# Performance work log

Measured on AMD Instinct MI355X. Metric: run time of the kernel, lower is better.

Reference implementation:

```python
import jax, jax.numpy as jnp
import numpy as np

B, S, H, NH = 32, 512, 768, 12
EC, EU = 4, 4
CAP = 1.0
DH = H // NH
CAPACITY = int(CAP * B / EC)  # Switch-style capacity per common expert


def setup_inputs() -> dict:
    key = jax.random.key(0)
    ks = jax.random.split(key, 10)
    s = 0.02
    E = EC + EU  # experts stacked: [0:EC]=common, [EC:]=unique
    return {
        "hidden_states": jax.random.normal(ks[0], (B, S, H), jnp.float32),
        "attention_mask": jnp.zeros((B, S), jnp.float32),  # additive mask
        "Wq": jax.random.normal(ks[1], (E, H, H), jnp.float32) * s,
        "bq": jnp.zeros((E, H), jnp.float32),
        "Wk": jax.random.normal(ks[2], (E, H, H), jnp.float32) * s,
        "bk": jnp.zeros((E, H), jnp.float32),
        "Wv": jax.random.normal(ks[3], (E, H, H), jnp.float32) * s,
        "bv": jnp.zeros((E, H), jnp.float32),
        "Wo": jax.random.normal(ks[4], (E, H, H), jnp.float32) * s,
        "bo": jnp.zeros((E, H), jnp.float32),
        "Wsc": jax.random.normal(ks[5], (H, EC), jnp.float32) * s,
        "bsc": jnp.zeros((EC,), jnp.float32),
        "Wsu": jax.random.normal(ks[6], (H, EU), jnp.float32) * s,
        "bsu": jnp.zeros((EU,), jnp.float32),
    }


def reference(hidden_states, attention_mask, Wq, bq, Wk, bk, Wv, bv, Wo, bo,
              Wsc, bsc, Wsu, bsu):
    # ---- common routing (per-sequence top-1 over mean-pooled tokens) ----
    h_mean = hidden_states.mean(axis=1)                       # [B,H]
    pc = jax.nn.softmax(h_mean @ Wsc + bsc, axis=-1)          # [B,EC]
    rc = jnp.argmax(pc, axis=-1)                              # [B]
    pc_max = jnp.max(pc, axis=-1)                             # [B]
    # capacity drop: within each expert keep the CAPACITY highest-prob seqs
    order = jnp.argsort(-pc_max)                              # global desc sort
    oh = jax.nn.one_hot(rc[order], EC, dtype=jnp.int32)       # [B,EC]
    rank = jnp.take_along_axis(jnp.cumsum(oh, axis=0), rc[order][:, None], 1)[:, 0]
    kept = jnp.zeros((B,), bool).at[order].set(rank <= CAPACITY)

    # ---- unique routing for dropped sequences (mean is per-sequence, so
    #      computing on the full batch and masking matches torch) ----
    pu = jax.nn.softmax(h_mean @ Wsu + bsu, axis=-1)          # [B,EU]
    ru = jnp.argmax(pu, axis=-1)
    pu_max = jnp.max(pu, axis=-1)

    # per-sequence expert index into stacked [EC+EU] expert params
    eidx = jnp.where(kept, rc, EC + ru)                       # [B]
    # scaling factor p/stop_grad(p): ==1 in fwd, routes grads to the gate
    scale = jnp.where(kept,
                      pc_max / jax.lax.stop_gradient(pc_max),
                      pu_max / jax.lax.stop_gradient(pu_max))

    # ---- gather-dispatch: per-sequence expert weights ----
    Wq_b, Wk_b, Wv_b, Wo_b = Wq[eidx], Wk[eidx], Wv[eidx], Wo[eidx]  # [B,H,H]
    bq_b, bk_b, bv_b, bo_b = bq[eidx], bk[eidx], bv[eidx], bo[eidx]  # [B,H]

    def heads(t):  # [B,S,H] -> [B,NH,S,DH]
        return t.reshape(B, S, NH, DH).transpose(0, 2, 1, 3)

    q = heads(jnp.einsum('bsh,bhd->bsd', hidden_states, Wq_b) + bq_b[:, None, :])
    k = heads(jnp.einsum('bsh,bhd->bsd', hidden_states, Wk_b) + bk_b[:, None, :])
    v = heads(jnp.einsum('bsh,bhd->bsd', hidden_states, Wv_b) + bv_b[:, None, :])

    scores = jnp.einsum('bhsd,bhtd->bhst', q, k) / np.float32(np.sqrt(DH))
    scores = scores + attention_mask[:, None, None, :]        # additive mask
    attn = jax.nn.softmax(scores, axis=-1)
    ctx = jnp.einsum('bhst,bhtd->bhsd', attn, v)
    ctx = ctx.transpose(0, 2, 1, 3).reshape(B, S, H)

    out = jnp.einsum('bsh,bhd->bsd', ctx, Wo_b) + bo_b[:, None, :]
    return out * scale[:, None, None]
```

## Files before the change

kernel.cpp:

```cpp
#include <hip/hip_runtime.h>
#include <hip/hip_bf16.h>

#define B_ 32
#define S_ 512
#define H_ 768
#define NH_ 12
#define DH_ 64
#define EC_ 4
#define CAPN_ 8

using short8  = __attribute__((ext_vector_type(8))) short;
using floatx4 = __attribute__((ext_vector_type(4))) float;
using uint2v  = __attribute__((ext_vector_type(2))) unsigned;
using bf16 = __hip_bfloat16;

#define VMCNT(n) asm volatile("s_waitcnt vmcnt(" #n ")" ::: "memory")

__device__ __forceinline__ void gl_lds16(const void* g, void* l) {
  __builtin_amdgcn_global_load_lds(
      (const __attribute__((address_space(1))) unsigned int*)g,
      (__attribute__((address_space(3))) unsigned int*)l, 16, 0, 0);
}

__device__ __forceinline__ unsigned pk2(float lo, float hi) {
  __hip_bfloat162 h = __float22bfloat162_rn(make_float2(lo, hi));
  unsigned r;
  __builtin_memcpy(&r, &h, 4);
  return r;
}

__global__ void k_prep(const float* __restrict__ X, bf16* __restrict__ Xh,
                       float* __restrict__ partial,
                       const float* __restrict__ Wq, const float* __restrict__ Wk,
                       const float* __restrict__ Wv, const float* __restrict__ Wo,
                       bf16* __restrict__ Wt) {
  __shared__ float tile[32][33];
  int f = blockIdx.x;
  if (f < 768) {
    int bx = f % 96, by = f / 96;
    int idx = bx * 256 + threadIdx.x;
    int b = idx / H_, h = idx - b * H_;
    int s0 = by * 64;
    size_t base = ((size_t)b * S_ + s0) * H_ + h;
    float sum = 0.f;
#pragma unroll 8
    for (int s = 0; s < 64; ++s) {
      float v = X[base + (size_t)s * H_];
      Xh[base + (size_t)s * H_] = __float2bfloat16(v);
      sum += v;
    }
    partial[(size_t)by * (B_ * H_) + idx] = sum;
  } else {
    int wid = f - 768;
    int z = wid / 576;
    int rem = wid - z * 576;
    int xx = rem / 24, yy = rem - xx * 24;
    const float* Wbase = (z < 8 ? Wq : z < 16 ? Wk : z < 24 ? Wv : Wo) + (size_t)(z & 7) * H_ * H_;
    int k0 = xx * 32, n0 = yy * 32;
    int tj = threadIdx.x & 31, ti = threadIdx.x >> 5;
#pragma unroll
    for (int r = 0; r < 4; ++r)
      tile[ti + r * 8][tj] = Wbase[(size_t)(k0 + ti + r * 8) * H_ + n0 + tj];
    __syncthreads();
    bf16* out = Wt + (size_t)z * H_ * H_;
#pragma unroll
    for (int r = 0; r < 4; ++r)
      out[(size_t)(n0 + ti + r * 8) * H_ + k0 + tj] = __float2bfloat16(tile[tj][ti + r * 8]);
  }
}

__global__ void k_mean_reduce(const float* __restrict__ partial, float* __restrict__ hmean) {
  int idx = blockIdx.x * 256 + threadIdx.x;
  float s = 0.f;
#pragma unroll
  for (int c = 0; c < 8; ++c) s += partial[(size_t)c * (B_ * H_) + idx];
  hmean[idx] = s * (1.f / 512.f);
}

__global__ void k_gate(const float* __restrict__ hmean,
                       const float* __restrict__ Wsc, const float* __restrict__ bsc,
                       const float* __restrict__ Wsu, const float* __restrict__ bsu,
                       float* __restrict__ logits) {
  int b = blockIdx.x;
  int t = threadIdx.x;
  int g = t >> 3, p = t & 7;
  const float* hm = hmean + (size_t)b * H_;
  const float* w;
  float bias;
  if (g < 4) { w = Wsc + g; bias = bsc[g]; }
  else       { w = Wsu + (g - 4); bias = bsu[g - 4]; }
  float acc = 0.f;
  for (int j = p; j < H_; j += 8) acc += hm[j] * w[j * 4];
  acc += __shfl_xor(acc, 1);
  acc += __shfl_xor(acc, 2);
  acc += __shfl_xor(acc, 4);
  if (p == 0) logits[b * 8 + g] = acc + bias;
}

__global__ void k_route2(const float* __restrict__ logits, int* __restrict__ eidx) {
  __shared__ float pcmax[B_];
  __shared__ int rc_s[B_], ru_s[B_];
  int t = threadIdx.x;
  if (t < B_) {
    float lg[8];
#pragma unroll
    for (int e = 0; e < 8; ++e) lg[e] = logits[t * 8 + e];
    float m = lg[0]; int a = 0;
    for (int e = 1; e < 4; ++e) if (lg[e] > m) { m = lg[e]; a = e; }
    float s = 0.f;
    for (int e = 0; e < 4; ++e) s += expf(lg[e] - m);
    pcmax[t] = 1.f / s;
    rc_s[t] = a;
    float mu = lg[4]; int au = 0;
    for (int e = 1; e < 4; ++e) if (lg[4 + e] > mu) { mu = lg[4 + e]; au = e; }
    ru_s[t] = au;
  }
  __syncthreads();
  if (t == 0) {
    bool used[B_], kept[B_];
    int cnt[EC_] = {0, 0, 0, 0};
    for (int i = 0; i < B_; ++i) used[i] = false;
    for (int i = 0; i < B_; ++i) {
      int best = 0; float bv = -1e30f;
      for (int j = 0; j < B_; ++j)
        if (!used[j] && pcmax[j] > bv) { bv = pcmax[j]; best = j; }
      used[best] = true;
      kept[best] = (++cnt[rc_s[best]] <= CAPN_);
    }
    for (int i = 0; i < B_; ++i)
      eidx[i] = kept[i] ? rc_s[i] : EC_ + ru_s[i];
  }
}

template <int OMODE, int NM>
__global__ __launch_bounds__(256, 2) void k_gemm(
    const bf16* __restrict__ A, const bf16* __restrict__ Wt,
    const float* __restrict__ bias0, const float* __restrict__ bias1,
    const float* __restrict__ bias2,
    void* out0, void* out1, void* out2,
    const int* __restrict__ eidx, int mat0) {
  __shared__ __align__(16) char ldsA[2][16384];
  __shared__ __align__(16) char ldsB[3][16384];
  const int nwg = 96 * NM * 8;
  int wg = blockIdx.x;
  int f = (wg & 7) * (nwg >> 3) + (wg >> 3);
  int b = f / (24 * NM);
  int r0 = f - b * 24 * NM;
  int mat = r0 / 24;
  int tile = r0 - mat * 24;
  int m0 = (tile & 3) * 128, n0 = (tile >> 2) * 128;
  int e = eidx[b];
  const bf16* Ab = A + (size_t)b * S_ * H_;
  const bf16* Wb = Wt + (size_t)((mat0 + mat) * 8 + e) * H_ * H_;
  const float* bias = ((mat == 0) ? bias0 : (mat == 1) ? bias1 : bias2) + (size_t)e * H_;
  void* outp = (mat == 0) ? out0 : (mat == 1) ? out1 : out2;

  int t = threadIdx.x, lane = t & 63, w = t >> 6;
  int wm = (w & 1) * 64, wn = (w >> 1) * 64;
  int lm = lane & 15, lq = lane >> 4;

  auto stageA = [&](char* buf, int kt) {
#pragma unroll
    for (int r = 0; r < 4; ++r) {
      int c = t + r * 256;
      int mm = c >> 3, pos = c & 7;
      int kc = pos ^ (mm & 7);
      gl_lds16(Ab + (size_t)(m0 + mm) * H_ + kt * 64 + kc * 8, buf + (size_t)c * 16);
    }
  };
  auto stageB = [&](char* buf, int kt) {
#pragma unroll
    for (int r = 0; r < 4; ++r) {
      int c = t + r * 256;
      int nn = c >> 3, pos = c & 7;
      int kc = pos ^ (nn & 7);
      gl_lds16(Wb + (size_t)(n0 + nn) * H_ + kt * 64 + kc * 8, buf + (size_t)c * 16);
    }
  };

  floatx4 acc[4][4] = {};
  stageA(ldsA[0], 0);
  stageB(ldsB[0], 0);
  stageB(ldsB[1], 1);
  VMCNT(4);
  __builtin_amdgcn_s_barrier();
  __builtin_amdgcn_sched_barrier(0);

  int bcur = 0, bstage = 2;
  for (int kt = 0; kt < 12; ++kt) {
    if (kt < 11) stageA(ldsA[(kt + 1) & 1], kt + 1);
    if (kt < 10) stageB(ldsB[bstage], kt + 2);
    const char* curA = ldsA[kt & 1];
    const char* curB = ldsB[bcur];
#pragma unroll
    for (int kf = 0; kf < 2; ++kf) {
      int kc = kf * 4 + lq;
      short8 af[4], bfr[4];
#pragma unroll
      for (int mf = 0; mf < 4; ++mf) {
        int mm = wm + mf * 16 + lm;
        af[mf] = *(const short8*)(curA + ((size_t)(mm * 8 + (kc ^ (mm & 7)))) * 16);
      }
#pragma unroll
      for (int nf = 0; nf < 4; ++nf) {
        int nn = wn + nf * 16 + lm;
        bfr[nf] = *(const short8*)(curB + ((size_t)(nn * 8 + (kc ^ (nn & 7)))) * 16);
      }
#pragma unroll
      for (int mf = 0; mf < 4; ++mf)
#pragma unroll
        for (int nf = 0; nf < 4; ++nf)
          acc[mf][nf] = __builtin_amdgcn_mfma_f32_16x16x32_bf16(af[mf], bfr[nf], acc[mf][nf], 0, 0, 0);
    }
    if (kt < 11) {
      if (kt < 10) { VMCNT(4); } else { VMCNT(0); }
      __builtin_amdgcn_s_barrier();
      __builtin_amdgcn_sched_barrier(0);
    }
    ++bcur; if (bcur == 3) bcur = 0;
    ++bstage; if (bstage == 3) bstage = 0;
  }

#pragma unroll
  for (int mf = 0; mf < 4; ++mf) {
#pragma unroll
    for (int nf = 0; nf < 4; ++nf) {
      int n = n0 + wn + nf * 16 + lm;
      float bv = bias[n];
      int mrow = m0 + wm + mf * 16 + lq * 4;
      size_t rowbase = ((size_t)b * S_ + mrow) * H_ + n;
#pragma unroll
      for (int r = 0; r < 4; ++r) {
        float v = acc[mf][nf][r] + bv;
        if (OMODE == 0) {
          if (mat == 2) {
            int s = mrow + r;
            ((bf16*)outp)[((size_t)(b * NH_ + (n >> 6))) * 32768 +
                          (size_t)(s >> 3) * 512 + (n & 63) * 8 + (s & 7)] =
                __float2bfloat16(v);
          } else {
            ((bf16*)outp)[rowbase + (size_t)r * H_] = __float2bfloat16(v);
          }
        } else {
          ((float*)outp)[rowbase + (size_t)r * H_] = v;
        }
      }
    }
  }
}

__global__ __launch_bounds__(256, 3) void k_attn(
    const bf16* __restrict__ Q, const bf16* __restrict__ K,
    const bf16* __restrict__ Vt, const float* __restrict__ mask,
    bf16* __restrict__ Ctx) {
  int bh = blockIdx.x;
  int b = bh / NH_, h = bh - b * NH_;
  int t = threadIdx.x, lane = t & 63, w = t >> 6;
  int lm = lane & 15, lq = lane >> 4;
  int q0 = blockIdx.y * 128 + w * 32;

  short8 qf[2][2];
#pragma unroll
  for (int mf = 0; mf < 2; ++mf)
#pragma unroll
    for (int kf = 0; kf < 2; ++kf)
      qf[mf][kf] = *(const short8*)(Q + ((size_t)(b * S_ + q0 + mf * 16 + lm)) * H_ +
                                    h * DH_ + kf * 32 + lq * 8);

  int kr = ((lm >> 2) << 3) + (lm & 3);
  const int koff[4] = {0, 4, 32, 36};
  const bf16* kbase = K + ((size_t)(b * S_) + kr) * H_ + h * DH_ + lq * 8;
  const bf16* vtb = Vt + ((size_t)(b * NH_ + h)) * 32768;
  const float* mbase = mask + (size_t)b * S_ + lq * 8;

  floatx4 oacc[2][4] = {};
  float m_[2] = {-1e30f, -1e30f}, l_[2] = {0.f, 0.f};

  for (int kt = 0; kt < 8; ++kt) {
    floatx4 sT[2][4] = {};
#pragma unroll
    for (int kf = 0; kf < 2; ++kf) {
      short8 kb4[4];
#pragma unroll
      for (int nf = 0; nf < 4; ++nf)
        kb4[nf] = *(const short8*)(kbase + (size_t)(kt * 64 + koff[nf]) * H_ + kf * 32);
#pragma unroll
      for (int mf = 0; mf < 2; ++mf)
#pragma unroll
        for (int nf = 0; nf < 4; ++nf)
          sT[mf][nf] = __builtin_amdgcn_mfma_f32_16x16x32_bf16(kb4[nf], qf[mf][kf], sT[mf][nf], 0, 0, 0);
    }
    short8 vf[2][4];
#pragma unroll
    for (int kf = 0; kf < 2; ++kf)
#pragma unroll
      for (int nf = 0; nf < 4; ++nf)
        vf[kf][nf] = *(const short8*)(vtb + (size_t)(kt * 8 + kf * 4 + lq) * 512 +
                                      (nf * 16 + lm) * 8);
    const floatx4* mp = (const floatx4*)(mbase + kt * 64);
    floatx4 mv[4] = {mp[0], mp[1], mp[8], mp[9]};

    short8 pf[2][2];
#pragma unroll
    for (int mf = 0; mf < 2; ++mf) {
      float p[4][4];
#pragma unroll
      for (int nf = 0; nf < 4; ++nf)
#pragma unroll
        for (int r = 0; r < 4; ++r)
          p[nf][r] = sT[mf][nf][r] * 0.125f + mv[nf][r];
      float t01 = fmaxf(fmaxf(fmaxf(p[0][0], p[0][1]), fmaxf(p[0][2], p[0][3])),
                        fmaxf(fmaxf(p[1][0], p[1][1]), fmaxf(p[1][2], p[1][3])));
      float t23 = fmaxf(fmaxf(fmaxf(p[2][0], p[2][1]), fmaxf(p[2][2], p[2][3])),
                        fmaxf(fmaxf(p[3][0], p[3][1]), fmaxf(p[3][2], p[3][3])));
      float tm = fmaxf(t01, t23);
      tm = fmaxf(tm, __shfl_xor(tm, 16));
      tm = fmaxf(tm, __shfl_xor(tm, 32));
      float mn = fmaxf(m_[mf], tm);
      float a = __expf(m_[mf] - mn);
      m_[mf] = mn;
      float ps = 0.f;
#pragma unroll
      for (int nf = 0; nf < 4; ++nf)
#pragma unroll
        for (int r = 0; r < 4; ++r) {
          p[nf][r] = __expf(p[nf][r] - mn);
          ps += p[nf][r];
        }
      ps += __shfl_xor(ps, 16);
      ps += __shfl_xor(ps, 32);
      l_[mf] = l_[mf] * a + ps;
#pragma unroll
      for (int nf = 0; nf < 4; ++nf) oacc[mf][nf] *= a;
      union { short8 s8; unsigned u[4]; } pku;
      pku.u[0] = pk2(p[0][0], p[0][1]); pku.u[1] = pk2(p[0][2], p[0][3]);
      pku.u[2] = pk2(p[1][0], p[1][1]); pku.u[3] = pk2(p[1][2], p[1][3]);
      pf[mf][0] = pku.s8;
      pku.u[0] = pk2(p[2][0], p[2][1]); pku.u[1] = pk2(p[2][2], p[2][3]);
      pku.u[2] = pk2(p[3][0], p[3][1]); pku.u[3] = pk2(p[3][2], p[3][3]);
      pf[mf][1] = pku.s8;
    }
#pragma unroll
    for (int kf = 0; kf < 2; ++kf)
#pragma unroll
      for (int mf = 0; mf < 2; ++mf)
#pragma unroll
        for (int nf = 0; nf < 4; ++nf)
          oacc[mf][nf] = __builtin_amdgcn_mfma_f32_16x16x32_bf16(vf[kf][nf], pf[mf][kf], oacc[mf][nf], 0, 0, 0);
  }
#pragma unroll
  for (int mf = 0; mf < 2; ++mf) {
    float inv = 1.f / l_[mf];
    bf16* op = Ctx + ((size_t)(b * S_ + q0 + mf * 16 + lm)) * H_ + h * DH_ + lq * 4;
#pragma unroll
    for (int nf = 0; nf < 4; ++nf) {
      uint2v o;
      o.x = pk2(oacc[mf][nf][0] * inv, oacc[mf][nf][1] * inv);
      o.y = pk2(oacc[mf][nf][2] * inv, oacc[mf][nf][3] * inv);
      *(uint2v*)(op + nf * 16) = o;
    }
  }
}

extern "C" void kernel_launch(void* const* d_in, const int* in_sizes, int n_in,
                              void* d_out, int out_size, void* d_ws, size_t ws_size,
                              hipStream_t stream) {
  const float* X    = (const float*)d_in[0];
  const float* mask = (const float*)d_in[1];
  const float* Wq   = (const float*)d_in[2];
  const float* bq   = (const float*)d_in[3];
  const float* Wk   = (const float*)d_in[4];
  const float* bk   = (const float*)d_in[5];
  const float* Wv   = (const float*)d_in[6];
  const float* bv   = (const float*)d_in[7];
  const float* Wo   = (const float*)d_in[8];
  const float* bo   = (const float*)d_in[9];
  const float* Wsc  = (const float*)d_in[10];
  const float* bsc  = (const float*)d_in[11];
  const float* Wsu  = (const float*)d_in[12];
  const float* bsu  = (const float*)d_in[13];

  char* ws = (char*)d_ws;
  int*   eidx    = (int*)ws;
  float* logits  = (float*)(ws + 128);
  float* partial = (float*)(ws + 1280);
  float* hmean   = (float*)(ws + 787712);
  bf16*  Xh      = (bf16*)(ws + 886016);
  bf16*  Wt      = (bf16*)(ws + 26051840);
  bf16*  qb      = (bf16*)(ws + 63800576);
  bf16*  kb      = (bf16*)(ws + 88966400);
  bf16*  Vt      = (bf16*)(ws + 114132224);
  bf16*  ctx     = Xh;

  k_prep<<<dim3(19200), 256, 0, stream>>>(X, Xh, partial, Wq, Wk, Wv, Wo, Wt);
  k_mean_reduce<<<96, 256, 0, stream>>>(partial, hmean);
  k_gate<<<B_, 64, 0, stream>>>(hmean, Wsc, bsc, Wsu, bsu, logits);
  k_route2<<<1, 64, 0, stream>>>(logits, eidx);
  k_gemm<0, 3><<<dim3(2304), 256, 0, stream>>>(Xh, Wt, bq, bk, bv,
                                               (void*)qb, (void*)kb, (void*)Vt, eidx, 0);
  k_attn<<<dim3(B_ * NH_, 4), 256, 0, stream>>>(qb, kb, Vt, mask, ctx);
  k_gemm<1, 1><<<dim3(768), 256, 0, stream>>>(ctx, Wt, bo, bo, bo,
                                              d_out, d_out, d_out, eidx, 3);
}
```

Before: 452.9 us.

## Load GEMM A operand directly into registers and raise occupancy to three blocks

The projection GEMM no longer stages the A (activation) tile through LDS. Each lane prefetches its A fragments straight from global memory into registers one k-step ahead, while B keeps its triple-buffered LDS pipeline. Dropping the A buffers frees 32KB of LDS per block, and the launch bound is raised to 3 workgroups per SIMD set to use that space for more occupancy. In exchange, A reads from global are less coalesced, there is more register pressure with a tighter VGPR cap, and the register copy of prefetched fragments may force extra waits that weaken the overlap.

Measured after the change: 521.3 us. 1.15x slower.

```diff
diff --git a/kernel.cpp b/kernel.cpp
--- a/kernel.cpp
+++ b/kernel.cpp
@@ -133,13 +133,12 @@
 }
 
 template <int OMODE, int NM>
-__global__ __launch_bounds__(256, 2) void k_gemm(
+__global__ __launch_bounds__(256, 3) void k_gemm(
     const bf16* __restrict__ A, const bf16* __restrict__ Wt,
     const float* __restrict__ bias0, const float* __restrict__ bias1,
     const float* __restrict__ bias2,
     void* out0, void* out1, void* out2,
     const int* __restrict__ eidx, int mat0) {
-  __shared__ __align__(16) char ldsA[2][16384];
   __shared__ __align__(16) char ldsB[3][16384];
   const int nwg = 96 * NM * 8;
   int wg = blockIdx.x;
@@ -159,15 +158,6 @@
   int wm = (w & 1) * 64, wn = (w >> 1) * 64;
   int lm = lane & 15, lq = lane >> 4;
 
-  auto stageA = [&](char* buf, int kt) {
-#pragma unroll
-    for (int r = 0; r < 4; ++r) {
-      int c = t + r * 256;
-      int mm = c >> 3, pos = c & 7;
-      int kc = pos ^ (mm & 7);
-      gl_lds16(Ab + (size_t)(m0 + mm) * H_ + kt * 64 + kc * 8, buf + (size_t)c * 16);
-    }
-  };
   auto stageB = [&](char* buf, int kt) {
 #pragma unroll
     for (int r = 0; r < 4; ++r) {
@@ -178,29 +168,36 @@
     }
   };
 
+  const bf16* arow[4];
+#pragma unroll
+  for (int mf = 0; mf < 4; ++mf)
+    arow[mf] = Ab + (size_t)(m0 + wm + mf * 16 + lm) * H_ + lq * 8;
+
+  short8 af[4][2], afn[4][2];
+  auto prefA = [&](short8 dst[4][2], int kt) {
+#pragma unroll
+    for (int mf = 0; mf < 4; ++mf)
+#pragma unroll
+      for (int kf = 0; kf < 2; ++kf)
+        dst[mf][kf] = *(const short8*)(arow[mf] + kt * 64 + kf * 32);
+  };
+
   floatx4 acc[4][4] = {};
-  stageA(ldsA[0], 0);
   stageB(ldsB[0], 0);
   stageB(ldsB[1], 1);
-  VMCNT(4);
+  prefA(af, 0);
+  VMCNT(8);
   __builtin_amdgcn_s_barrier();
   __builtin_amdgcn_sched_barrier(0);
 
-  int bcur = 0, bstage = 2;
   for (int kt = 0; kt < 12; ++kt) {
-    if (kt < 11) stageA(ldsA[(kt + 1) & 1], kt + 1);
-    if (kt < 10) stageB(ldsB[bstage], kt + 2);
-    const char* curA = ldsA[kt & 1];
-    const char* curB = ldsB[bcur];
+    if (kt < 10) stageB(ldsB[(kt + 2) % 3], kt + 2);
+    if (kt < 11) prefA(afn, kt + 1);
+    const char* curB = ldsB[kt % 3];
 #pragma unroll
     for (int kf = 0; kf < 2; ++kf) {
       int kc = kf * 4 + lq;
-      short8 af[4], bfr[4];
-#pragma unroll
-      for (int mf = 0; mf < 4; ++mf) {
-        int mm = wm + mf * 16 + lm;
-        af[mf] = *(const short8*)(curA + ((size_t)(mm * 8 + (kc ^ (mm & 7)))) * 16);
-      }
+      short8 bfr[4];
 #pragma unroll
       for (int nf = 0; nf < 4; ++nf) {
         int nn = wn + nf * 16 + lm;
@@ -210,15 +207,18 @@
       for (int mf = 0; mf < 4; ++mf)
 #pragma unroll
         for (int nf = 0; nf < 4; ++nf)
-          acc[mf][nf] = __builtin_amdgcn_mfma_f32_16x16x32_bf16(af[mf], bfr[nf], acc[mf][nf], 0, 0, 0);
-    }
+          acc[mf][nf] = __builtin_amdgcn_mfma_f32_16x16x32_bf16(af[mf][kf], bfr[nf], acc[mf][nf], 0, 0, 0);
+    }
+#pragma unroll
+    for (int mf = 0; mf < 4; ++mf)
+#pragma unroll
+      for (int kf = 0; kf < 2; ++kf)
+        af[mf][kf] = afn[mf][kf];
     if (kt < 11) {
-      if (kt < 10) { VMCNT(4); } else { VMCNT(0); }
+      VMCNT(12);
       __builtin_amdgcn_s_barrier();
       __builtin_amdgcn_sched_barrier(0);
     }
-    ++bcur; if (bcur == 3) bcur = 0;
-    ++bstage; if (bstage == 3) bstage = 0;
   }
 
 #pragma unroll
```
